# Kernel optimization log

Measured on AMD Instinct MI355X. Metric: run time of the kernel, lower is better.

Reference implementation:

```python
import jax, jax.numpy as jnp
import numpy as np

N_LOC, C_SIZE, A_SIZE, CTRL_IN = 8192, 2048, 512, 1024
D_FULL = C_SIZE + A_SIZE  # 2560
EPS = 1e-7


def setup_inputs() -> dict:
    key = jax.random.key(0)
    ks = jax.random.split(key, 16)
    s = 0.02  # stand-in for xavier init scale
    return {
        "controller_hidden_state": jax.random.normal(ks[0], (N_LOC, 1), jnp.float32),
        "controller_input": jax.random.normal(ks[1], (CTRL_IN, 1), jnp.float32),
        "memory_contents": jax.random.normal(ks[2], (N_LOC, C_SIZE), jnp.float32) * s,
        "memory_addresses": jax.random.normal(ks[3], (N_LOC, A_SIZE), jnp.float32) * s,
        "exp_mov_avg_similarity": jax.random.normal(ks[4], (N_LOC, 1), jnp.float32) * s,
        "W_query": jax.random.normal(ks[5], (D_FULL, N_LOC), jnp.float32) * s,
        "b_query": jax.random.normal(ks[6], (D_FULL, 1), jnp.float32) * s,
        "u_sharpen": jax.random.normal(ks[7], (1, N_LOC), jnp.float32) * s,
        "b_sharpen": jax.random.normal(ks[8], (1,), jnp.float32) * s,
        "u_lru": jax.random.normal(ks[9], (1, N_LOC), jnp.float32) * s,
        "b_lru": jax.random.normal(ks[10], (1,), jnp.float32) * s,
        "W_erase": jax.random.normal(ks[11], (C_SIZE, N_LOC), jnp.float32) * s,
        "b_erase": jax.random.normal(ks[12], (C_SIZE, 1), jnp.float32) * s,
        "W_content_hidden": jax.random.normal(ks[13], (C_SIZE, N_LOC), jnp.float32) * s,
        "W_content_input": jax.random.normal(ks[14], (C_SIZE, CTRL_IN), jnp.float32) * s,
        "u_content_alpha": jax.random.normal(ks[15], (1, N_LOC + CTRL_IN), jnp.float32) * s,
        "b_content_alpha": jnp.zeros((1,), jnp.float32),
    }


def reference(controller_hidden_state, controller_input, memory_contents,
              memory_addresses, exp_mov_avg_similarity, W_query, b_query,
              u_sharpen, b_sharpen, u_lru, b_lru, W_erase, b_erase,
              W_content_hidden, W_content_input, u_content_alpha,
              b_content_alpha):
    h, x = controller_hidden_state, controller_input
    full_mem = jnp.concatenate([memory_addresses, memory_contents], axis=1)  # [N, D]

    # --- addressing ---
    query = W_query @ h + b_query                                   # [D, 1]
    beta = jax.nn.softplus(u_sharpen @ h + b_sharpen) + 1.0         # [1, 1]
    q = query[:, 0]
    dots = full_mem @ q                                             # [N]
    q_norm = jnp.maximum(jnp.linalg.norm(q), EPS)
    m_norm = jnp.maximum(jnp.linalg.norm(full_mem, axis=1), EPS)
    sim = (beta[0, 0] * dots / (m_norm * q_norm))[:, None]          # [N, 1]

    gamma = jax.nn.sigmoid(u_lru @ h + b_lru)                       # [1, 1]
    address = jax.nn.softmax(sim - gamma * exp_mov_avg_similarity, axis=0)  # [N, 1]
    new_ema = 0.1 * exp_mov_avg_similarity + 0.9 * sim

    # --- read (uses pre-update memory; last location excluded as in source) ---
    read_vec = full_mem[:-1].T @ address[:-1]                       # [D, 1]

    # --- update: erase + write, vectorized rank-1 update over locations ---
    erase = W_erase @ h + b_erase                                   # [C, 1]
    alpha = u_content_alpha @ jnp.concatenate([h, x], axis=0) + b_content_alpha  # [1, 1]
    cand = jax.nn.relu(W_content_hidden @ h + alpha * (W_content_input @ x))     # [C, 1]
    new_mem = memory_contents + address * (cand - erase).T          # [N, C]

    return read_vec, new_mem, address, new_ema
```

## Files before the change

kernel.cpp:

```cpp
#include <hip/hip_runtime.h>
#include <hip/hip_bf16.h>
#include <math.h>

#define N_LOC   8192
#define C_SIZE  2048
#define A_SIZE  512
#define CTRL_IN 1024
#define D_FULL  2560
#define EPS_F   1e-7f
#define NCHUNK  128

typedef float f4 __attribute__((ext_vector_type(4)));

__device__ __forceinline__ f4 nt4(const f4* p) { return __builtin_nontemporal_load(p); }
__device__ __forceinline__ float hsum4(f4 v) { return v.x + v.y + v.z + v.w; }

__device__ __forceinline__ float waveReduceSum(float v) {
    #pragma unroll
    for (int off = 32; off > 0; off >>= 1) v += __shfl_xor(v, off, 64);
    return v;
}
__device__ __forceinline__ float waveReduceMax(float v) {
    #pragma unroll
    for (int off = 32; off > 0; off >>= 1) v = fmaxf(v, __shfl_xor(v, off, 64));
    return v;
}

__global__ __launch_bounds__(256) void k_matvec(
    const float* __restrict__ h, const float* __restrict__ x,
    const float* __restrict__ Wq, const float* __restrict__ bq,
    const float* __restrict__ We, const float* __restrict__ be,
    const float* __restrict__ Wch, const float* __restrict__ Wci,
    float* __restrict__ q_out, float* __restrict__ erase_out,
    float* __restrict__ wh_out, float* __restrict__ wx_out)
{
    __shared__ float red[4];
    int tid  = threadIdx.x;
    int lane = tid & 63;
    int wid  = tid >> 6;
    int blk  = blockIdx.x;

    float acc;
    float bias = 0.f;
    float* out;

    if (blk < 6656) {
        const float* W;
        if (blk < 2560)      { int r = blk;        W = Wq  + (size_t)r * 8192; bias = bq[r]; out = q_out + r; }
        else if (blk < 4608) { int r = blk - 2560; W = We  + (size_t)r * 8192; bias = be[r]; out = erase_out + r; }
        else                 { int r = blk - 4608; W = Wch + (size_t)r * 8192; out = wh_out + r; }

        const f4* W4 = (const f4*)W;
        const f4* h4 = (const f4*)h;
        f4 w[8], v[8];
        #pragma unroll
        for (int u = 0; u < 8; ++u) w[u] = nt4(W4 + tid + 256 * u);
        #pragma unroll
        for (int u = 0; u < 8; ++u) v[u] = h4[tid + 256 * u];
        f4 a4 = w[0] * v[0];
        #pragma unroll
        for (int u = 1; u < 8; ++u) a4 += w[u] * v[u];
        acc = hsum4(a4);
    } else {
        int r = blk - 6656;
        const f4* W4 = (const f4*)(Wci + (size_t)r * 1024);
        const f4* x4 = (const f4*)x;
        f4 w = nt4(W4 + tid);
        f4 v = x4[tid];
        acc = hsum4(w * v);
        out = wx_out + r;
    }

    acc = waveReduceSum(acc);
    if (lane == 0) red[wid] = acc;
    __syncthreads();
    if (tid == 0) *out = red[0] + red[1] + red[2] + red[3] + bias;
}

__global__ void k_rowpass(const float* __restrict__ ma, const float* __restrict__ mc,
                          const float* __restrict__ q,
                          float* __restrict__ dotb, float* __restrict__ ssqb)
{
    int wave = (blockIdx.x * blockDim.x + threadIdx.x) >> 6;
    int lane = threadIdx.x & 63;
    if (wave >= N_LOC) return;
    int row = wave;

    const f4* a4 = (const f4*)(ma + (size_t)row * A_SIZE);
    const f4* c4 = (const f4*)(mc + (size_t)row * C_SIZE);
    const f4* q4 = (const f4*)q;

    f4 dv = {0.f, 0.f, 0.f, 0.f}, sv = {0.f, 0.f, 0.f, 0.f};
    #pragma unroll
    for (int i = lane; i < 128; i += 64) {
        f4 v = a4[i], qq = q4[i];
        dv += v * qq;
        sv += v * v;
    }
    #pragma unroll
    for (int i = lane; i < 512; i += 64) {
        f4 v = c4[i], qq = q4[128 + i];
        dv += v * qq;
        sv += v * v;
    }
    float dot = waveReduceSum(hsum4(dv));
    float ssq = waveReduceSum(hsum4(sv));
    if (lane == 0) {
        dotb[row] = dot;
        ssqb[row] = ssq;
    }
}

__global__ __launch_bounds__(1024) void k_fuse(
    const float* __restrict__ h, const float* __restrict__ x,
    const float* __restrict__ us, const float* __restrict__ bs,
    const float* __restrict__ ul, const float* __restrict__ bl,
    const float* __restrict__ uca, const float* __restrict__ bca,
    const float* __restrict__ q, const float* __restrict__ erase,
    const float* __restrict__ wh, const float* __restrict__ wx,
    const float* __restrict__ dotb, const float* __restrict__ ssqb,
    const float* __restrict__ ema,
    float* __restrict__ addr_out, float* __restrict__ newema_out,
    float* __restrict__ cdiff)
{
    __shared__ float red[16];
    __shared__ float s_beta, s_gamma, s_qn, s_alpha, s_max, s_sum;
    int tid = threadIdx.x, lane = tid & 63, wid = tid >> 6;

    float a_us = 0.f, a_ul = 0.f, a_a = 0.f, a_q2 = 0.f;
    for (int i = tid; i < 8192; i += 1024) {
        float hv = h[i];
        a_us += us[i] * hv;
        a_ul += ul[i] * hv;
        a_a  += uca[i] * hv;
    }
    a_a += uca[8192 + tid] * x[tid];
    for (int i = tid; i < 2560; i += 1024) { float qv = q[i]; a_q2 += qv * qv; }

    float vals[4] = { a_us, a_ul, a_a, a_q2 };
    float res[4];
    #pragma unroll
    for (int k = 0; k < 4; ++k) {
        float v = waveReduceSum(vals[k]);
        __syncthreads();
        if (lane == 0) red[wid] = v;
        __syncthreads();
        float r = 0.f;
        if (tid == 0) { for (int i = 0; i < 16; ++i) r += red[i]; }
        res[k] = r;
    }
    if (tid == 0) {
        float z = res[0] + bs[0];
        float sp = (z > 20.f) ? z : log1pf(expf(z));
        s_beta  = sp + 1.0f;
        s_gamma = 1.f / (1.f + expf(-(res[1] + bl[0])));
        s_alpha = res[2] + bca[0];
        s_qn    = fmaxf(sqrtf(res[3]), EPS_F);
    }
    __syncthreads();

    float beta = s_beta, gamma = s_gamma, qn = s_qn;
    float v[8];
    float lmax = -INFINITY;
    #pragma unroll
    for (int k = 0; k < 8; ++k) {
        int r = tid + k * 1024;
        float d  = dotb[r];
        float sq = ssqb[r];
        float e  = ema[r];
        float mn  = fmaxf(sqrtf(sq), EPS_F);
        float sim = beta * d / (mn * qn);
        v[k] = sim - gamma * e;
        newema_out[r] = 0.1f * e + 0.9f * sim;
        lmax = fmaxf(lmax, v[k]);
    }

    lmax = waveReduceMax(lmax);
    __syncthreads();
    if (lane == 0) red[wid] = lmax;
    __syncthreads();
    if (tid == 0) { float m = red[0]; for (int i = 1; i < 16; ++i) m = fmaxf(m, red[i]); s_max = m; }
    __syncthreads();
    float m = s_max, lsum = 0.f;
    #pragma unroll
    for (int k = 0; k < 8; ++k) { v[k] = expf(v[k] - m); lsum += v[k]; }
    lsum = waveReduceSum(lsum);
    __syncthreads();
    if (lane == 0) red[wid] = lsum;
    __syncthreads();
    if (tid == 0) { float s = 0.f; for (int i = 0; i < 16; ++i) s += red[i]; s_sum = s; }
    __syncthreads();
    float inv = 1.f / s_sum;
    #pragma unroll
    for (int k = 0; k < 8; ++k) addr_out[tid + k * 1024] = v[k] * inv;

    float al = s_alpha;
    for (int j = tid; j < 2048; j += 1024) {
        float cand = fmaxf(wh[j] + al * wx[j], 0.f);
        cdiff[j] = cand - erase[j];
    }
}

__global__ void k_colpass(const float* __restrict__ ma, const float* __restrict__ mc,
                          const float* __restrict__ addr, const float* __restrict__ cdiff,
                          float* __restrict__ newmem_out, float* __restrict__ rvpart)
{
    int c     = blockIdx.x * 256 + threadIdx.x;
    int chunk = blockIdx.y;
    const int RPC = N_LOC / NCHUNK;
    int r0 = chunk * RPC, r1 = r0 + RPC;

    float acc = 0.f;
    if (c < A_SIZE) {
        const float* p = ma + c;
        for (int r = r0; r < r1; ++r) {
            float val = p[(size_t)r * A_SIZE];
            float a = addr[r];
            if (r != N_LOC - 1) acc += a * val;
        }
    } else {
        int cc = c - A_SIZE;
        float cd = cdiff[cc];
        const float* p = mc + cc;
        float* o = newmem_out + cc;
        for (int r = r0; r < r1; ++r) {
            float val = p[(size_t)r * C_SIZE];
            float a = addr[r];
            if (r != N_LOC - 1) acc += a * val;
            o[(size_t)r * C_SIZE] = val + a * cd;
        }
    }
    rvpart[(size_t)chunk * D_FULL + c] = acc;
}

__global__ void k_rvreduce(const float* __restrict__ rvpart, float* __restrict__ rv_out)
{
    int c = blockIdx.x * 256 + threadIdx.x;
    if (c >= D_FULL) return;
    float s = 0.f;
    for (int k = 0; k < NCHUNK; ++k) s += rvpart[(size_t)k * D_FULL + c];
    rv_out[c] = s;
}

extern "C" void kernel_launch(void* const* d_in, const int* in_sizes, int n_in,
                              void* d_out, int out_size, void* d_ws, size_t ws_size,
                              hipStream_t stream)
{
    const float* h   = (const float*)d_in[0];
    const float* x   = (const float*)d_in[1];
    const float* mc  = (const float*)d_in[2];
    const float* ma  = (const float*)d_in[3];
    const float* ema = (const float*)d_in[4];
    const float* Wq  = (const float*)d_in[5];
    const float* bq  = (const float*)d_in[6];
    const float* us  = (const float*)d_in[7];
    const float* bs  = (const float*)d_in[8];
    const float* ul  = (const float*)d_in[9];
    const float* bl  = (const float*)d_in[10];
    const float* We  = (const float*)d_in[11];
    const float* be  = (const float*)d_in[12];
    const float* Wch = (const float*)d_in[13];
    const float* Wci = (const float*)d_in[14];
    const float* uca = (const float*)d_in[15];
    const float* bca = (const float*)d_in[16];

    float* out = (float*)d_out;
    float* rv_out     = out;
    float* newmem_out = out + D_FULL;
    float* addr_out   = newmem_out + (size_t)N_LOC * C_SIZE;
    float* newema_out = addr_out + N_LOC;

    float* ws = (float*)d_ws;
    float* w_query = ws;
    float* w_erase = ws + 2560;
    float* w_wh    = ws + 4608;
    float* w_wx    = ws + 6656;
    float* w_cdiff = ws + 8704;
    float* w_dot   = ws + 10752;
    float* w_ssq   = ws + 18944;
    float* w_rvp   = ws + 27136;

    k_matvec<<<8704, 256, 0, stream>>>(h, x, Wq, bq, We, be, Wch, Wci,
                                       w_query, w_erase, w_wh, w_wx);
    k_rowpass<<<2048, 256, 0, stream>>>(ma, mc, w_query, w_dot, w_ssq);
    k_fuse<<<1, 1024, 0, stream>>>(h, x, us, bs, ul, bl, uca, bca,
                                   w_query, w_erase, w_wh, w_wx,
                                   w_dot, w_ssq, ema,
                                   addr_out, newema_out, w_cdiff);
    dim3 g5(D_FULL / 256, NCHUNK);
    k_colpass<<<g5, 256, 0, stream>>>(ma, mc, addr_out, w_cdiff, newmem_out, w_rvp);
    k_rvreduce<<<10, 256, 0, stream>>>(w_rvp, rv_out);
}
```

Baseline: 99.72 us.

## Split query matvec out and fuse row pass with remaining matvecs

The query matvec now runs alone first. The per-row dot/norm pass is merged with the erase, content-hidden and content-input matvecs into one interleaved kernel, with the block role picked by blockIdx & 3. The goal is to remove the serial dependency where the row pass waited for all matvecs to finish, so independent memory streams overlap within one launch. In exchange the memory rows are now read alongside the weight streams rather than just before the column pass, which could change cache reuse for the later memory read.

```diff
diff --git a/kernel.cpp b/kernel.cpp
--- a/kernel.cpp
+++ b/kernel.cpp
@@ -26,89 +26,110 @@
     return v;
 }
 
-__global__ __launch_bounds__(256) void k_matvec(
-    const float* __restrict__ h, const float* __restrict__ x,
+
+__global__ __launch_bounds__(256) void k_query(
+    const float* __restrict__ h,
     const float* __restrict__ Wq, const float* __restrict__ bq,
+    float* __restrict__ q_out)
+{
+    __shared__ float red[4];
+    int tid  = threadIdx.x;
+    int lane = tid & 63;
+    int wid  = tid >> 6;
+    int r    = blockIdx.x;
+
+    const f4* W4 = (const f4*)(Wq + (size_t)r * 8192);
+    const f4* h4 = (const f4*)h;
+    f4 w[8], v[8];
+    #pragma unroll
+    for (int u = 0; u < 8; ++u) w[u] = nt4(W4 + tid + 256 * u);
+    #pragma unroll
+    for (int u = 0; u < 8; ++u) v[u] = h4[tid + 256 * u];
+    f4 a4 = w[0] * v[0];
+    #pragma unroll
+    for (int u = 1; u < 8; ++u) a4 += w[u] * v[u];
+    float acc = waveReduceSum(hsum4(a4));
+    if (lane == 0) red[wid] = acc;
+    __syncthreads();
+    if (tid == 0) q_out[r] = red[0] + red[1] + red[2] + red[3] + bq[r];
+}
+
+__global__ __launch_bounds__(256) void k_stream(
+    const float* __restrict__ ma, const float* __restrict__ mc,
+    const float* __restrict__ q,  const float* __restrict__ h,
+    const float* __restrict__ x,
     const float* __restrict__ We, const float* __restrict__ be,
     const float* __restrict__ Wch, const float* __restrict__ Wci,
-    float* __restrict__ q_out, float* __restrict__ erase_out,
-    float* __restrict__ wh_out, float* __restrict__ wx_out)
+    float* __restrict__ dotb, float* __restrict__ ssqb,
+    float* __restrict__ erase_out, float* __restrict__ wh_out,
+    float* __restrict__ wx_out)
 {
     __shared__ float red[4];
     int tid  = threadIdx.x;
     int lane = tid & 63;
     int wid  = tid >> 6;
     int blk  = blockIdx.x;
-
-    float acc;
-    float bias = 0.f;
-    float* out;
-
-    if (blk < 6656) {
-        const float* W;
-        if (blk < 2560)      { int r = blk;        W = Wq  + (size_t)r * 8192; bias = bq[r]; out = q_out + r; }
-        else if (blk < 4608) { int r = blk - 2560; W = We  + (size_t)r * 8192; bias = be[r]; out = erase_out + r; }
-        else                 { int r = blk - 4608; W = Wch + (size_t)r * 8192; out = wh_out + r; }
-
-        const f4* W4 = (const f4*)W;
-        const f4* h4 = (const f4*)h;
-        f4 w[8], v[8];
+    int sub  = blk & 3;
+    int idx  = blk >> 2;
+
+    if (sub == 0) {
+        int row = idx * 4 + wid;
+        const f4* a4 = (const f4*)(ma + (size_t)row * A_SIZE);
+        const f4* c4 = (const f4*)(mc + (size_t)row * C_SIZE);
+        const f4* q4 = (const f4*)q;
+
+        f4 dv = {0.f, 0.f, 0.f, 0.f}, sv = {0.f, 0.f, 0.f, 0.f};
         #pragma unroll
-        for (int u = 0; u < 8; ++u) w[u] = nt4(W4 + tid + 256 * u);
+        for (int i = lane; i < 128; i += 64) {
+            f4 v = a4[i], qq = q4[i];
+            dv += v * qq;
+            sv += v * v;
+        }
         #pragma unroll
-        for (int u = 0; u < 8; ++u) v[u] = h4[tid + 256 * u];
-        f4 a4 = w[0] * v[0];
-        #pragma unroll
-        for (int u = 1; u < 8; ++u) a4 += w[u] * v[u];
-        acc = hsum4(a4);
-    } else {
-        int r = blk - 6656;
-        const f4* W4 = (const f4*)(Wci + (size_t)r * 1024);
+        for (int i = lane; i < 512; i += 64) {
+            f4 v = c4[i], qq = q4[128 + i];
+            dv += v * qq;
+            sv += v * v;
+        }
+        float dot = waveReduceSum(hsum4(dv));
+        float ssq = waveReduceSum(hsum4(sv));
+        if (lane == 0) {
+            dotb[row] = dot;
+            ssqb[row] = ssq;
+        }
+        return;
+    }
+
+    if (sub == 3) {
+        const f4* W4 = (const f4*)(Wci + (size_t)idx * 1024);
         const f4* x4 = (const f4*)x;
         f4 w = nt4(W4 + tid);
         f4 v = x4[tid];
-        acc = hsum4(w * v);
-        out = wx_out + r;
-    }
-
-    acc = waveReduceSum(acc);
+        float acc = waveReduceSum(hsum4(w * v));
+        if (lane == 0) red[wid] = acc;
+        __syncthreads();
+        if (tid == 0) wx_out[idx] = red[0] + red[1] + red[2] + red[3];
+        return;
+    }
+
+    const float* W; float bias = 0.f; float* out;
+    if (sub == 1) { W = We  + (size_t)idx * 8192; bias = be[idx]; out = erase_out + idx; }
+    else          { W = Wch + (size_t)idx * 8192;                 out = wh_out + idx; }
+
+    const f4* W4 = (const f4*)W;
+    const f4* h4 = (const f4*)h;
+    f4 w[8], v[8];
+    #pragma unroll
+    for (int u = 0; u < 8; ++u) w[u] = nt4(W4 + tid + 256 * u);
+    #pragma unroll
+    for (int u = 0; u < 8; ++u) v[u] = h4[tid + 256 * u];
+    f4 a4 = w[0] * v[0];
+    #pragma unroll
+    for (int u = 1; u < 8; ++u) a4 += w[u] * v[u];
+    float acc = waveReduceSum(hsum4(a4));
     if (lane == 0) red[wid] = acc;
     __syncthreads();
     if (tid == 0) *out = red[0] + red[1] + red[2] + red[3] + bias;
-}
-
-__global__ void k_rowpass(const float* __restrict__ ma, const float* __restrict__ mc,
-                          const float* __restrict__ q,
-                          float* __restrict__ dotb, float* __restrict__ ssqb)
-{
-    int wave = (blockIdx.x * blockDim.x + threadIdx.x) >> 6;
-    int lane = threadIdx.x & 63;
-    if (wave >= N_LOC) return;
-    int row = wave;
-
-    const f4* a4 = (const f4*)(ma + (size_t)row * A_SIZE);
-    const f4* c4 = (const f4*)(mc + (size_t)row * C_SIZE);
-    const f4* q4 = (const f4*)q;
-
-    f4 dv = {0.f, 0.f, 0.f, 0.f}, sv = {0.f, 0.f, 0.f, 0.f};
-    #pragma unroll
-    for (int i = lane; i < 128; i += 64) {
-        f4 v = a4[i], qq = q4[i];
-        dv += v * qq;
-        sv += v * v;
-    }
-    #pragma unroll
-    for (int i = lane; i < 512; i += 64) {
-        f4 v = c4[i], qq = q4[128 + i];
-        dv += v * qq;
-        sv += v * v;
-    }
-    float dot = waveReduceSum(hsum4(dv));
-    float ssq = waveReduceSum(hsum4(sv));
-    if (lane == 0) {
-        dotb[row] = dot;
-        ssqb[row] = ssq;
-    }
 }
 
 __global__ __launch_bounds__(1024) void k_fuse(
@@ -280,9 +301,9 @@
     float* w_ssq   = ws + 18944;
     float* w_rvp   = ws + 27136;
 
-    k_matvec<<<8704, 256, 0, stream>>>(h, x, Wq, bq, We, be, Wch, Wci,
-                                       w_query, w_erase, w_wh, w_wx);
-    k_rowpass<<<2048, 256, 0, stream>>>(ma, mc, w_query, w_dot, w_ssq);
+    k_query<<<2560, 256, 0, stream>>>(h, Wq, bq, w_query);
+    k_stream<<<8192, 256, 0, stream>>>(ma, mc, w_query, h, x, We, be, Wch, Wci,
+                                       w_dot, w_ssq, w_erase, w_wh, w_wx);
     k_fuse<<<1, 1024, 0, stream>>>(h, x, us, bs, ul, bl, uca, bca,
                                    w_query, w_erase, w_wh, w_wx,
                                    w_dot, w_ssq, ema,
```

Measured after the change: 103.7 us. 4.0% more time.
